# Performance work log

Hardware: AMD Instinct MI355X
Metric: run time of the kernel (lower is better)

The kernel has to match this reference:

```python
import jax, jax.numpy as jnp
import numpy as np

B, T, C, H = 4, 2048, 1024, 16
D = C // H  # head_dim = 64

def setup_inputs() -> dict:
    key = jax.random.key(0)
    ks = jax.random.split(key, 5)
    scale = 1.0 / np.sqrt(C)
    return {
        "x": jax.random.normal(ks[0], (B, T, C), dtype=jnp.float32),
        "Wq": jax.random.normal(ks[1], (C, C), dtype=jnp.float32) * scale,
        "Wk": jax.random.normal(ks[2], (C, C), dtype=jnp.float32) * scale,
        "Wv": jax.random.normal(ks[3], (C, C), dtype=jnp.float32) * scale,
        "Wo": jax.random.normal(ks[4], (C, C), dtype=jnp.float32) * scale,
        "bo": jnp.zeros((C,), dtype=jnp.float32),
    }

def reference(x, Wq, Wk, Wv, Wo, bo):
    Bx, Tx, Cx = x.shape
    # projections -> [B, H, T, D]
    def split_heads(y):
        return y.reshape(Bx, Tx, H, D).transpose(0, 2, 1, 3)
    Q = split_heads(x @ Wq)
    K = split_heads(x @ Wk)
    V = split_heads(x @ Wv)
    # scaled dot-product with causal mask: [B, H, T, T]
    scores = jnp.einsum('bhqd,bhkd->bhqk', Q, K) / jnp.sqrt(jnp.asarray(D, x.dtype))
    causal = jnp.tril(jnp.ones((Tx, Tx), dtype=bool))
    scores = jnp.where(causal, scores, -jnp.inf)
    weights = jax.nn.softmax(scores, axis=-1)
    attn = jnp.einsum('bhqk,bhkd->bhqd', weights, V)  # [B, H, T, D]
    out = attn.transpose(0, 2, 1, 3).reshape(Bx, Tx, Cx)
    return out @ Wo + bo
```

## Files before the change

kernel.cpp:

```cpp
#include <hip/hip_runtime.h>
#include <hip/hip_bf16.h>
#include <cmath>

typedef __bf16 bf16;
typedef __bf16 bf16x8 __attribute__((ext_vector_type(8)));
typedef __bf16 bf16x4v __attribute__((ext_vector_type(4)));
typedef float f32x4 __attribute__((ext_vector_type(4)));

#define B_ 4
#define T_ 2048
#define C_ 1024
#define H_ 16
#define D_ 64
#define BT_ 8192
#define LOG2E 1.4426950408889634f

__device__ __forceinline__ void async_cp16(const void* g, void* l) {
  __builtin_amdgcn_global_load_lds(
      (__attribute__((address_space(1))) void*)g,
      (__attribute__((address_space(3))) void*)l, 16, 0, 0);
}

__device__ __forceinline__ f32x4 mfma16(bf16x8 a, bf16x8 b, f32x4 c) {
  return __builtin_amdgcn_mfma_f32_16x16x32_bf16(a, b, c, 0, 0, 0);
}

__global__ __launch_bounds__(256) void prep_kernel(
    const float* __restrict__ x, const float* __restrict__ Wq,
    const float* __restrict__ Wk, const float* __restrict__ Wv,
    const float* __restrict__ Wo, bf16* __restrict__ xb,
    bf16* __restrict__ wt) {
  __shared__ float tile[32][33];
  const int id = blockIdx.x;
  const int t = threadIdx.x;
  if (id < 8192) {
    const int i = id * 256 + t;
    float4 v = ((const float4*)x)[i];
    bf16x4v o = {(bf16)v.x, (bf16)v.y, (bf16)v.z, (bf16)v.w};
    ((bf16x4v*)xb)[i] = o;
    return;
  }
  const int id2 = id - 8192;
  const int z = id2 >> 10;
  const float* W = (z == 0) ? Wq : (z == 1) ? Wk : (z == 2) ? Wv : Wo;
  bf16* Wt = wt + (size_t)z * 1048576;
  const int bx = id2 & 31, by = (id2 >> 5) & 31;
  const int xx = t & 31, yy = t >> 5;
  const int n0 = bx * 32, k0 = by * 32;
#pragma unroll
  for (int j = 0; j < 32; j += 8)
    tile[yy + j][xx] = W[(size_t)(k0 + yy + j) * C_ + n0 + xx];
  __syncthreads();
#pragma unroll
  for (int j = 0; j < 32; j += 8)
    Wt[(size_t)(n0 + yy + j) * C_ + k0 + xx] = (bf16)tile[xx][yy + j];
}

template <int F32OUT>
__device__ __forceinline__ void gemm_tile_sb(
    const bf16* __restrict__ A, const bf16* __restrict__ Bt,
    void* __restrict__ Cv, const float* __restrict__ bias, int M, int N, int K,
    int m0, int n0, bf16* As, bf16* Bs) {
  const int t = threadIdx.x;
  const int lane = t & 63;
  const int wave = t >> 6;
  const int quad = lane >> 4;
  const int l15 = lane & 15;
  const int l7 = l15 & 7;
  const int wm = (wave >> 1) * 64;
  const int wn = (wave & 1) * 64;

  const int sr8 = lane >> 3;
  const int sc = (lane & 7) ^ sr8;
  const bf16* Ag = A + (size_t)(m0 + wave * 32 + sr8) * K + sc * 8;
  const bf16* Bg = Bt + (size_t)(n0 + wave * 32 + sr8) * K + sc * 8;

  const int niter = K >> 6;
  auto stage = [&](int kt) {
    bf16* Ad = As + wave * 2048 + lane * 8;
    bf16* Bd = Bs + wave * 2048 + lane * 8;
#pragma unroll
    for (int i = 0; i < 4; i++) {
      async_cp16(Ag + kt * 64 + (size_t)(i * 8) * K, Ad + i * 512);
      async_cp16(Bg + kt * 64 + (size_t)(i * 8) * K, Bd + i * 512);
    }
  };

  f32x4 acc[4][4] = {};

  for (int kt = 0; kt < niter; kt++) {
    if (kt) __syncthreads();
    stage(kt);
    __syncthreads();
#pragma unroll
    for (int ks = 0; ks < 2; ks++) {
      bf16x8 af[4], bfr[4];
#pragma unroll
      for (int i = 0; i < 4; i++)
        af[i] = *(const bf16x8*)&As[(wm + i * 16 + l15) * 64 +
                                    (((ks * 4 + quad) ^ l7) * 8)];
#pragma unroll
      for (int j = 0; j < 4; j++)
        bfr[j] = *(const bf16x8*)&Bs[(wn + j * 16 + l15) * 64 +
                                     (((ks * 4 + quad) ^ l7) * 8)];
#pragma unroll
      for (int i = 0; i < 4; i++)
#pragma unroll
        for (int j = 0; j < 4; j++)
          acc[i][j] = mfma16(af[i], bfr[j], acc[i][j]);
    }
  }

#pragma unroll
  for (int i = 0; i < 4; i++) {
    const int gr = m0 + wm + i * 16 + quad * 4;
#pragma unroll
    for (int j = 0; j < 4; j++) {
      const int gc = n0 + wn + j * 16 + l15;
      const float bv = F32OUT ? bias[gc] : 0.0f;
#pragma unroll
      for (int r = 0; r < 4; r++) {
        const float v = acc[i][j][r] + bv;
        if (F32OUT)
          ((float*)Cv)[(size_t)(gr + r) * N + gc] = v;
        else
          ((bf16*)Cv)[(size_t)(gr + r) * N + gc] = (bf16)v;
      }
    }
  }
}

template <int F32OUT>
__device__ __forceinline__ void gemm_tile_db(
    const bf16* __restrict__ A, const bf16* __restrict__ Bt,
    void* __restrict__ Cv, const float* __restrict__ bias, int M, int N, int K,
    int m0, int n0, bf16* As, bf16* Bs) {
  const int t = threadIdx.x;
  const int lane = t & 63;
  const int wave = t >> 6;
  const int quad = lane >> 4;
  const int l15 = lane & 15;
  const int l7 = l15 & 7;
  const int wm = (wave >> 1) * 64;
  const int wn = (wave & 1) * 64;

  const int sr8 = lane >> 3;
  const int sc = (lane & 7) ^ sr8;
  const bf16* Ag = A + (size_t)(m0 + wave * 32 + sr8) * K + sc * 8;
  const bf16* Bg = Bt + (size_t)(n0 + wave * 32 + sr8) * K + sc * 8;

  const int niter = K >> 6;
  auto stage = [&](int kt, int buf) {
    bf16* Ad = As + buf * 8192 + wave * 2048 + lane * 8;
    bf16* Bd = Bs + buf * 8192 + wave * 2048 + lane * 8;
#pragma unroll
    for (int i = 0; i < 4; i++) {
      async_cp16(Ag + kt * 64 + (size_t)(i * 8) * K, Ad + i * 512);
      async_cp16(Bg + kt * 64 + (size_t)(i * 8) * K, Bd + i * 512);
    }
  };

  f32x4 acc[4][4] = {};
  stage(0, 0);

  for (int kt = 0; kt < niter; kt++) {
    __syncthreads();
    if (kt + 1 < niter) stage(kt + 1, (kt + 1) & 1);
    const bf16* Ab = As + (kt & 1) * 8192;
    const bf16* Bb = Bs + (kt & 1) * 8192;
#pragma unroll
    for (int ks = 0; ks < 2; ks++) {
      bf16x8 af[4], bfr[4];
#pragma unroll
      for (int i = 0; i < 4; i++)
        af[i] = *(const bf16x8*)&Ab[(wm + i * 16 + l15) * 64 +
                                    (((ks * 4 + quad) ^ l7) * 8)];
#pragma unroll
      for (int j = 0; j < 4; j++)
        bfr[j] = *(const bf16x8*)&Bb[(wn + j * 16 + l15) * 64 +
                                     (((ks * 4 + quad) ^ l7) * 8)];
#pragma unroll
      for (int i = 0; i < 4; i++)
#pragma unroll
        for (int j = 0; j < 4; j++)
          acc[i][j] = mfma16(af[i], bfr[j], acc[i][j]);
    }
  }

#pragma unroll
  for (int i = 0; i < 4; i++) {
    const int gr = m0 + wm + i * 16 + quad * 4;
#pragma unroll
    for (int j = 0; j < 4; j++) {
      const int gc = n0 + wn + j * 16 + l15;
      const float bv = F32OUT ? bias[gc] : 0.0f;
#pragma unroll
      for (int r = 0; r < 4; r++) {
        const float v = acc[i][j][r] + bv;
        if (F32OUT)
          ((float*)Cv)[(size_t)(gr + r) * N + gc] = v;
        else
          ((bf16*)Cv)[(size_t)(gr + r) * N + gc] = (bf16)v;
      }
    }
  }
}

__global__ __launch_bounds__(256, 4) void qkv_gemm_kernel(
    const bf16* __restrict__ xb, const bf16* __restrict__ wqkvT,
    bf16* __restrict__ qkb, bf16* __restrict__ vtb) {
  __shared__ __align__(16) bf16 As[8192];
  __shared__ __align__(16) bf16 Bs[8192];
  int id = blockIdx.x;
  if (id < 1024) {
    gemm_tile_sb<0>(xb, wqkvT, (void*)qkb, nullptr, 8192, 2048, 1024,
                    (id >> 4) * 128, (id & 15) * 128, As, Bs);
  } else {
    id -= 1024;
    gemm_tile_sb<0>(wqkvT + 2 * 1024 * 1024, xb, (void*)vtb, nullptr, 1024,
                    8192, 1024, (id >> 6) * 128, (id & 63) * 128, As, Bs);
  }
}

__global__ __launch_bounds__(256, 2) void out_gemm_kernel(
    const bf16* __restrict__ attn, const bf16* __restrict__ woT,
    float* __restrict__ out, const float* __restrict__ bo) {
  __shared__ __align__(16) bf16 As[2 * 8192];
  __shared__ __align__(16) bf16 Bs[2 * 8192];
  const int id = blockIdx.x;
  gemm_tile_db<1>(attn, woT, (void*)out, bo, 8192, 1024, 1024,
                  (id >> 3) * 128, (id & 7) * 128, As, Bs);
}

__constant__ int QTPERM[16] = {15, 14, 13, 12, 8, 9, 10, 11,
                               7,  6,  5,  4,  0, 1, 2,  3};

__global__ __launch_bounds__(256, 4) void flash_attn_kernel(
    const bf16* __restrict__ qk, const bf16* __restrict__ vt,
    bf16* __restrict__ attn) {
  __shared__ __align__(16) char smem[34816];
  bf16* Ks = (bf16*)smem;
  bf16* Vs = (bf16*)(smem + 8192);
  bf16* Ps = (bf16*)(smem + 16384);

  const int t = threadIdx.x;
  const int lane = t & 63;
  const int wave = t >> 6;
  const int quad = lane >> 4;
  const int l15 = lane & 15;
  const int l7 = l15 & 7;
  const int bx = blockIdx.x;
  const int qt = QTPERM[bx >> 6];
  const int bh = bx & 63;
  const int b = bh >> 4;
  const int h = bh & 15;

  const bf16* Qg = qk + (size_t)b * T_ * 2048 + h * 64;
  const bf16* Kg = qk + (size_t)b * T_ * 2048 + 1024 + h * 64;
  const bf16* Vg = vt + (size_t)h * 64 * BT_ + b * T_;

  const float QSCALE = 0.125f * LOG2E;
  bf16x8 qf[2][2];
  const int qrow0 = qt * 128 + wave * 32;
#pragma unroll
  for (int mt = 0; mt < 2; mt++)
#pragma unroll
    for (int ks = 0; ks < 2; ks++) {
      bf16x8 v = *(const bf16x8*)(Qg + (size_t)(qrow0 + mt * 16 + l15) * 2048 +
                                  ks * 32 + quad * 8);
#pragma unroll
      for (int j = 0; j < 8; j++) v[j] = (bf16)((float)v[j] * QSCALE);
      qf[mt][ks] = v;
    }

  f32x4 o_acc[4][2] = {};
  f32x4 l4[2] = {};

  const int sr8 = lane >> 3;
  const int sc = (lane & 7) ^ sr8;

  auto stage = [&](int j64) {
    const int k0 = j64 * 64;
    bf16* KL = Ks + wave * 1024 + lane * 8;
    const bf16* KG = Kg + (size_t)(k0 + wave * 16 + sr8) * 2048 + sc * 8;
    async_cp16(KG, KL);
    async_cp16(KG + (size_t)8 * 2048, KL + 512);
    bf16* VL = Vs + wave * 1024 + lane * 8;
    const bf16* VG = Vg + (size_t)(wave * 16 + sr8) * BT_ + k0 + sc * 8;
    async_cp16(VG, VL);
    async_cp16(VG + (size_t)8 * BT_, VL + 512);
  };

  const int S = 2 * qt + 2;

  for (int s = 0; s < S; s++) {
    if (s) __syncthreads();
    stage(s);
    __syncthreads();
    const int k0 = s * 64;
    const bool diag = (s >= 2 * qt);

    bf16x4v p[2][4];
#pragma unroll
    for (int kt = 0; kt < 4; kt++) {
      const bf16x8 kf0 =
          *(const bf16x8*)&Ks[(kt * 16 + l15) * 64 + ((quad ^ l7) * 8)];
      const bf16x8 kf1 =
          *(const bf16x8*)&Ks[(kt * 16 + l15) * 64 + (((4 + quad) ^ l7) * 8)];
#pragma unroll
      for (int mt = 0; mt < 2; mt++) {
        __builtin_amdgcn_s_setprio(1);
        f32x4 sv = mfma16(kf0, qf[mt][0], f32x4{0.f, 0.f, 0.f, 0.f});
        sv = mfma16(kf1, qf[mt][1], sv);
        __builtin_amdgcn_s_setprio(0);
        if (diag) {
          const int qg = qt * 128 + wave * 32 + mt * 16 + l15;
#pragma unroll
          for (int i = 0; i < 4; i++)
            if (k0 + kt * 16 + quad * 4 + i > qg) sv[i] = -INFINITY;
        }
        f32x4 e;
#pragma unroll
        for (int i = 0; i < 4; i++) e[i] = __builtin_amdgcn_exp2f(sv[i]);
        l4[mt] += e;
        p[mt][kt] = bf16x4v{(bf16)e[0], (bf16)e[1], (bf16)e[2], (bf16)e[3]};
      }
    }

#pragma unroll
    for (int mt = 0; mt < 2; mt++) {
      const int row = wave * 32 + mt * 16 + l15;
#pragma unroll
      for (int kt = 0; kt < 4; kt++)
        *(bf16x4v*)&Ps[row * 72 + kt * 16 + quad * 4] = p[mt][kt];
    }

#pragma unroll
    for (int ks2 = 0; ks2 < 2; ks2++) {
      bf16x8 pa[2], vb[4];
#pragma unroll
      for (int mt = 0; mt < 2; mt++)
        pa[mt] = *(const bf16x8*)&Ps[(wave * 32 + mt * 16 + l15) * 72 +
                                     ks2 * 32 + quad * 8];
#pragma unroll
      for (int dt = 0; dt < 4; dt++)
        vb[dt] = *(const bf16x8*)&Vs[(dt * 16 + l15) * 64 +
                                     (((ks2 * 4 + quad) ^ l7) * 8)];
      __builtin_amdgcn_s_setprio(1);
#pragma unroll
      for (int dt = 0; dt < 4; dt++)
#pragma unroll
        for (int mt = 0; mt < 2; mt++)
          o_acc[dt][mt] = mfma16(vb[dt], pa[mt], o_acc[dt][mt]);
      __builtin_amdgcn_s_setprio(0);
    }
  }

  float inv[2];
#pragma unroll
  for (int mt = 0; mt < 2; mt++) {
    float l = l4[mt][0] + l4[mt][1] + l4[mt][2] + l4[mt][3];
    l += __shfl_xor(l, 16, 64);
    l += __shfl_xor(l, 32, 64);
    inv[mt] = 1.0f / l;
  }
#pragma unroll
  for (int dt = 0; dt < 4; dt++)
#pragma unroll
    for (int mt = 0; mt < 2; mt++) {
      const int q = qt * 128 + wave * 32 + mt * 16 + l15;
      bf16x4v o = {(bf16)(o_acc[dt][mt][0] * inv[mt]),
                   (bf16)(o_acc[dt][mt][1] * inv[mt]),
                   (bf16)(o_acc[dt][mt][2] * inv[mt]),
                   (bf16)(o_acc[dt][mt][3] * inv[mt])};
      *(bf16x4v*)(attn + (size_t)(b * T_ + q) * 1024 + h * 64 + dt * 16 +
                  quad * 4) = o;
    }
}

extern "C" void kernel_launch(void* const* d_in, const int* in_sizes, int n_in,
                              void* d_out, int out_size, void* d_ws,
                              size_t ws_size, hipStream_t stream) {
  const float* x = (const float*)d_in[0];
  const float* Wq = (const float*)d_in[1];
  const float* Wk = (const float*)d_in[2];
  const float* Wv = (const float*)d_in[3];
  const float* Wo = (const float*)d_in[4];
  const float* bo = (const float*)d_in[5];
  float* out = (float*)d_out;

  char* ws = (char*)d_ws;
  bf16* xb = (bf16*)(ws);
  bf16* qkb = (bf16*)(ws + 16777216);
  bf16* vtb = (bf16*)(ws + 50331648);
  bf16* attn = (bf16*)(ws + 67108864);
  bf16* wqkvT = (bf16*)(ws + 83886080);

  prep_kernel<<<12288, 256, 0, stream>>>(x, Wq, Wk, Wv, Wo, xb, wqkvT);

  qkv_gemm_kernel<<<1536, 256, 0, stream>>>(xb, wqkvT, qkb, vtb);

  flash_attn_kernel<<<1024, 256, 0, stream>>>(qkb, vtb, attn);

  out_gemm_kernel<<<512, 256, 0, stream>>>(attn, wqkvT + 3 * 1024 * 1024, out,
                                           bo);
}
```

Measured before the change: 235.6 us.

## Double-buffer K/V tiles and use per-wave compact P scratch in flash attention

The K/V shared-memory staging becomes double-buffered. The next tile's async global-to-LDS copies are issued right after the barrier, so they overlap the current tile's QK^T, softmax and PV work, and one barrier per iteration is removed. The shared P staging buffer shrinks to a per-wave 16x36 scratch that is written and immediately re-read per 32-key half and per m-tile, which cuts LDS footprint and the distance between write and read. Costs are more LDS per block, which could pressure 4-block occupancy, and 16-byte LDS reads at a 72-byte row stride that may not be 16-byte aligned.

```diff
diff --git a/kernel.cpp b/kernel.cpp
--- a/kernel.cpp
+++ b/kernel.cpp
@@ -238,10 +238,10 @@
 __global__ __launch_bounds__(256, 4) void flash_attn_kernel(
     const bf16* __restrict__ qk, const bf16* __restrict__ vt,
     bf16* __restrict__ attn) {
-  __shared__ __align__(16) char smem[34816];
-  bf16* Ks = (bf16*)smem;
-  bf16* Vs = (bf16*)(smem + 8192);
-  bf16* Ps = (bf16*)(smem + 16384);
+  __shared__ __align__(16) char smem[37376];
+  bf16* KsB = (bf16*)smem;
+  bf16* VsB = (bf16*)(smem + 16384);
+  bf16* Ps = (bf16*)(smem + 32768);
 
   const int t = threadIdx.x;
   const int lane = t & 63;
@@ -259,6 +259,8 @@
   const bf16* Kg = qk + (size_t)b * T_ * 2048 + 1024 + h * 64;
   const bf16* Vg = vt + (size_t)h * 64 * BT_ + b * T_;
 
+  bf16* Psw = Ps + wave * 576;
+
   const float QSCALE = 0.125f * LOG2E;
   bf16x8 qf[2][2];
   const int qrow0 = qt * 128 + wave * 32;
@@ -279,24 +281,26 @@
   const int sr8 = lane >> 3;
   const int sc = (lane & 7) ^ sr8;
 
-  auto stage = [&](int j64) {
+  auto stage = [&](int j64, int buf) {
     const int k0 = j64 * 64;
-    bf16* KL = Ks + wave * 1024 + lane * 8;
+    bf16* KL = KsB + buf * 4096 + wave * 1024 + lane * 8;
     const bf16* KG = Kg + (size_t)(k0 + wave * 16 + sr8) * 2048 + sc * 8;
     async_cp16(KG, KL);
     async_cp16(KG + (size_t)8 * 2048, KL + 512);
-    bf16* VL = Vs + wave * 1024 + lane * 8;
+    bf16* VL = VsB + buf * 4096 + wave * 1024 + lane * 8;
     const bf16* VG = Vg + (size_t)(wave * 16 + sr8) * BT_ + k0 + sc * 8;
     async_cp16(VG, VL);
     async_cp16(VG + (size_t)8 * BT_, VL + 512);
   };
 
   const int S = 2 * qt + 2;
+  stage(0, 0);
 
   for (int s = 0; s < S; s++) {
-    if (s) __syncthreads();
-    stage(s);
     __syncthreads();
+    if (s + 1 < S) stage(s + 1, (s + 1) & 1);
+    const bf16* Kb = KsB + (s & 1) * 4096;
+    const bf16* Vb = VsB + (s & 1) * 4096;
     const int k0 = s * 64;
     const bool diag = (s >= 2 * qt);
 
@@ -304,9 +308,9 @@
 #pragma unroll
     for (int kt = 0; kt < 4; kt++) {
       const bf16x8 kf0 =
-          *(const bf16x8*)&Ks[(kt * 16 + l15) * 64 + ((quad ^ l7) * 8)];
+          *(const bf16x8*)&Kb[(kt * 16 + l15) * 64 + ((quad ^ l7) * 8)];
       const bf16x8 kf1 =
-          *(const bf16x8*)&Ks[(kt * 16 + l15) * 64 + (((4 + quad) ^ l7) * 8)];
+          *(const bf16x8*)&Kb[(kt * 16 + l15) * 64 + (((4 + quad) ^ l7) * 8)];
 #pragma unroll
       for (int mt = 0; mt < 2; mt++) {
         __builtin_amdgcn_s_setprio(1);
@@ -328,31 +332,23 @@
     }
 
 #pragma unroll
-    for (int mt = 0; mt < 2; mt++) {
-      const int row = wave * 32 + mt * 16 + l15;
-#pragma unroll
-      for (int kt = 0; kt < 4; kt++)
-        *(bf16x4v*)&Ps[row * 72 + kt * 16 + quad * 4] = p[mt][kt];
-    }
-
-#pragma unroll
-    for (int ks2 = 0; ks2 < 2; ks2++) {
-      bf16x8 pa[2], vb[4];
-#pragma unroll
-      for (int mt = 0; mt < 2; mt++)
-        pa[mt] = *(const bf16x8*)&Ps[(wave * 32 + mt * 16 + l15) * 72 +
-                                     ks2 * 32 + quad * 8];
+    for (int hh = 0; hh < 2; hh++) {
+      bf16x8 vb[4];
 #pragma unroll
       for (int dt = 0; dt < 4; dt++)
-        vb[dt] = *(const bf16x8*)&Vs[(dt * 16 + l15) * 64 +
-                                     (((ks2 * 4 + quad) ^ l7) * 8)];
-      __builtin_amdgcn_s_setprio(1);
-#pragma unroll
-      for (int dt = 0; dt < 4; dt++)
-#pragma unroll
-        for (int mt = 0; mt < 2; mt++)
-          o_acc[dt][mt] = mfma16(vb[dt], pa[mt], o_acc[dt][mt]);
-      __builtin_amdgcn_s_setprio(0);
+        vb[dt] = *(const bf16x8*)&Vb[(dt * 16 + l15) * 64 +
+                                     (((hh * 4 + quad) ^ l7) * 8)];
+#pragma unroll
+      for (int mt = 0; mt < 2; mt++) {
+        *(bf16x4v*)&Psw[l15 * 36 + quad * 4] = p[mt][2 * hh];
+        *(bf16x4v*)&Psw[l15 * 36 + 16 + quad * 4] = p[mt][2 * hh + 1];
+        const bf16x8 pa = *(const bf16x8*)&Psw[l15 * 36 + quad * 8];
+        __builtin_amdgcn_s_setprio(1);
+#pragma unroll
+        for (int dt = 0; dt < 4; dt++)
+          o_acc[dt][mt] = mfma16(vb[dt], pa, o_acc[dt][mt]);
+        __builtin_amdgcn_s_setprio(0);
+      }
     }
   }
 
```

After: 249.8 us. 1.06x slower.

## Use 128x64 single-buffered tiles for output projection GEMM

Applied to the files above, without the earlier changes.

Replaces the double-buffered 128x128 output-projection GEMM tile with a single-buffered 128x64 tile, doubling the grid from 512 to 1024 blocks and raising the occupancy hint from 2 to 4 blocks per CU. The goal is to fill the 256 CUs better: 512 blocks is only two per CU, leaving the machine underused. In exchange each block gets less operand reuse per load and loses the overlap of the next tile's loads with current MFMAs, since it now synchronises twice per k-step.

```diff
diff --git a/kernel.cpp b/kernel.cpp
--- a/kernel.cpp
+++ b/kernel.cpp
@@ -130,57 +130,54 @@
   }
 }
 
-template <int F32OUT>
-__device__ __forceinline__ void gemm_tile_db(
+__device__ __forceinline__ void gemm_tile_sb64(
     const bf16* __restrict__ A, const bf16* __restrict__ Bt,
-    void* __restrict__ Cv, const float* __restrict__ bias, int M, int N, int K,
-    int m0, int n0, bf16* As, bf16* Bs) {
+    float* __restrict__ C, const float* __restrict__ bias, int M, int N,
+    int K, int m0, int n0, bf16* As, bf16* Bs) {
   const int t = threadIdx.x;
   const int lane = t & 63;
   const int wave = t >> 6;
   const int quad = lane >> 4;
   const int l15 = lane & 15;
   const int l7 = l15 & 7;
-  const int wm = (wave >> 1) * 64;
-  const int wn = (wave & 1) * 64;
+  const int wm = wave * 32;
 
   const int sr8 = lane >> 3;
   const int sc = (lane & 7) ^ sr8;
   const bf16* Ag = A + (size_t)(m0 + wave * 32 + sr8) * K + sc * 8;
-  const bf16* Bg = Bt + (size_t)(n0 + wave * 32 + sr8) * K + sc * 8;
+  const bf16* Bg = Bt + (size_t)(n0 + wave * 16 + sr8) * K + sc * 8;
 
   const int niter = K >> 6;
-  auto stage = [&](int kt, int buf) {
-    bf16* Ad = As + buf * 8192 + wave * 2048 + lane * 8;
-    bf16* Bd = Bs + buf * 8192 + wave * 2048 + lane * 8;
-#pragma unroll
-    for (int i = 0; i < 4; i++) {
+  auto stage = [&](int kt) {
+    bf16* Ad = As + wave * 2048 + lane * 8;
+    bf16* Bd = Bs + wave * 1024 + lane * 8;
+#pragma unroll
+    for (int i = 0; i < 4; i++)
       async_cp16(Ag + kt * 64 + (size_t)(i * 8) * K, Ad + i * 512);
+#pragma unroll
+    for (int i = 0; i < 2; i++)
       async_cp16(Bg + kt * 64 + (size_t)(i * 8) * K, Bd + i * 512);
-    }
   };
 
-  f32x4 acc[4][4] = {};
-  stage(0, 0);
+  f32x4 acc[2][4] = {};
 
   for (int kt = 0; kt < niter; kt++) {
+    if (kt) __syncthreads();
+    stage(kt);
     __syncthreads();
-    if (kt + 1 < niter) stage(kt + 1, (kt + 1) & 1);
-    const bf16* Ab = As + (kt & 1) * 8192;
-    const bf16* Bb = Bs + (kt & 1) * 8192;
 #pragma unroll
     for (int ks = 0; ks < 2; ks++) {
-      bf16x8 af[4], bfr[4];
-#pragma unroll
-      for (int i = 0; i < 4; i++)
-        af[i] = *(const bf16x8*)&Ab[(wm + i * 16 + l15) * 64 +
+      bf16x8 af[2], bfr[4];
+#pragma unroll
+      for (int i = 0; i < 2; i++)
+        af[i] = *(const bf16x8*)&As[(wm + i * 16 + l15) * 64 +
                                     (((ks * 4 + quad) ^ l7) * 8)];
 #pragma unroll
       for (int j = 0; j < 4; j++)
-        bfr[j] = *(const bf16x8*)&Bb[(wn + j * 16 + l15) * 64 +
+        bfr[j] = *(const bf16x8*)&Bs[(j * 16 + l15) * 64 +
                                      (((ks * 4 + quad) ^ l7) * 8)];
 #pragma unroll
-      for (int i = 0; i < 4; i++)
+      for (int i = 0; i < 2; i++)
 #pragma unroll
         for (int j = 0; j < 4; j++)
           acc[i][j] = mfma16(af[i], bfr[j], acc[i][j]);
@@ -188,20 +185,15 @@
   }
 
 #pragma unroll
-  for (int i = 0; i < 4; i++) {
+  for (int i = 0; i < 2; i++) {
     const int gr = m0 + wm + i * 16 + quad * 4;
 #pragma unroll
     for (int j = 0; j < 4; j++) {
-      const int gc = n0 + wn + j * 16 + l15;
-      const float bv = F32OUT ? bias[gc] : 0.0f;
-#pragma unroll
-      for (int r = 0; r < 4; r++) {
-        const float v = acc[i][j][r] + bv;
-        if (F32OUT)
-          ((float*)Cv)[(size_t)(gr + r) * N + gc] = v;
-        else
-          ((bf16*)Cv)[(size_t)(gr + r) * N + gc] = (bf16)v;
-      }
+      const int gc = n0 + j * 16 + l15;
+      const float bv = bias[gc];
+#pragma unroll
+      for (int r = 0; r < 4; r++)
+        C[(size_t)(gr + r) * N + gc] = acc[i][j][r] + bv;
     }
   }
 }
@@ -222,14 +214,14 @@
   }
 }
 
-__global__ __launch_bounds__(256, 2) void out_gemm_kernel(
+__global__ __launch_bounds__(256, 4) void out_gemm_kernel(
     const bf16* __restrict__ attn, const bf16* __restrict__ woT,
     float* __restrict__ out, const float* __restrict__ bo) {
-  __shared__ __align__(16) bf16 As[2 * 8192];
-  __shared__ __align__(16) bf16 Bs[2 * 8192];
+  __shared__ __align__(16) bf16 As[8192];
+  __shared__ __align__(16) bf16 Bs[4096];
   const int id = blockIdx.x;
-  gemm_tile_db<1>(attn, woT, (void*)out, bo, 8192, 1024, 1024,
-                  (id >> 3) * 128, (id & 7) * 128, As, Bs);
+  gemm_tile_sb64(attn, woT, out, bo, 8192, 1024, 1024, (id >> 4) * 128,
+                 (id & 15) * 64, As, Bs);
 }
 
 __constant__ int QTPERM[16] = {15, 14, 13, 12, 8, 9, 10, 11,
@@ -402,6 +394,6 @@
 
   flash_attn_kernel<<<1024, 256, 0, stream>>>(qkb, vtb, attn);
 
-  out_gemm_kernel<<<512, 256, 0, stream>>>(attn, wqkvT + 3 * 1024 * 1024, out,
-                                           bo);
-}
+  out_gemm_kernel<<<1024, 256, 0, stream>>>(attn, wqkvT + 3 * 1024 * 1024,
+                                            out, bo);
+}
```

New measurement: 233.3 us. No clear change (-1.0%).
